# Kernel optimization log

Measured on AMD Instinct MI355X. Metric: run time of the kernel, lower is better.

The kernel has to match this reference:

```python
import jax, jax.numpy as jnp
import numpy as np

N = 50000      # nodes
E = 800000     # edges (avg degree 16)
IN = 128       # in_channels
H = 8          # heads (layer 1)
C = 32         # hidden_channels per head
OUT = 40       # out_channels + 1
NEG_SLOPE = 0.2  # PyG GATConv default


def glorot(key, shape, fan_in, fan_out):
    lim = np.sqrt(6.0 / (fan_in + fan_out)).astype(np.float32)
    return jax.random.uniform(key, shape, jnp.float32, -lim, lim)


def setup_inputs() -> dict:
    key = jax.random.key(0)
    ks = jax.random.split(key, 10)
    x = jax.random.normal(ks[0], (N, IN), jnp.float32)
    edge_index = jax.random.randint(ks[1], (2, E), 0, N, dtype=jnp.int32)
    # layer 1: in -> H*C, heads=8, concat
    W1 = glorot(ks[2], (IN, H * C), IN, H * C)
    att_src1 = glorot(ks[3], (H, C), C, C)
    att_dst1 = glorot(ks[4], (H, C), C, C)
    b1 = jnp.zeros((H * C,), jnp.float32)
    # layer 2: H*C -> OUT, heads=1
    W2 = glorot(ks[5], (H * C, OUT), H * C, OUT)
    att_src2 = glorot(ks[6], (1, OUT), OUT, OUT)
    att_dst2 = glorot(ks[7], (1, OUT), OUT, OUT)
    b2 = jnp.zeros((OUT,), jnp.float32)
    return {"x": x, "edge_index": edge_index, "W1": W1, "att_src1": att_src1,
            "att_dst1": att_dst1, "b1": b1, "W2": W2, "att_src2": att_src2,
            "att_dst2": att_dst2, "b2": b2}


def gat_conv(x, edge_index, W, att_src, att_dst, bias):
    # PyG GATConv (eval mode, add_self_loops=True, concat=True)
    n = x.shape[0]
    heads, ch = att_src.shape
    loop = jnp.arange(n, dtype=edge_index.dtype)
    src = jnp.concatenate([edge_index[0], loop])  # message source j
    dst = jnp.concatenate([edge_index[1], loop])  # message target i
    h = (x @ W).reshape(n, heads, ch)                       # [N,H,C]
    a_src = jnp.einsum('nhc,hc->nh', h, att_src)            # [N,H]
    a_dst = jnp.einsum('nhc,hc->nh', h, att_dst)            # [N,H]
    logits = jax.nn.leaky_relu(a_src[src] + a_dst[dst], NEG_SLOPE)  # [Et,H]
    # segmented softmax over incoming edges of each target node
    m = jax.ops.segment_max(logits, dst, num_segments=n)    # [N,H]
    p = jnp.exp(logits - m[dst])
    s = jax.ops.segment_sum(p, dst, num_segments=n)         # [N,H]
    alpha = p / s[dst]                                      # [Et,H]
    msg = h[src] * alpha[:, :, None]                        # [Et,H,C]
    out = jax.ops.segment_sum(msg, dst, num_segments=n)     # [N,H,C]
    return out.reshape(n, heads * ch) + bias


def reference(x, edge_index, W1, att_src1, att_dst1, b1, W2, att_src2, att_dst2, b2):
    h = gat_conv(x, edge_index, W1, att_src1, att_dst1, b1)
    h = jax.nn.relu(h)  # dropout is identity in eval mode
    h = gat_conv(h, edge_index, W2, att_src2, att_dst2, b2)
    return jax.nn.log_softmax(h, axis=1)
```

## Files before the change

kernel.cpp:

```cpp
#include <hip/hip_runtime.h>
#include <hip/hip_bf16.h>
#include <math.h>

#define NEG_SLOPE 0.2f

__device__ __forceinline__ float lrelu(float x){ return x > 0.f ? x : NEG_SLOPE * x; }
__device__ __forceinline__ unsigned short f2bf(float f){
  __hip_bfloat16 h = __float2bfloat16(f);
  return __builtin_bit_cast(unsigned short, h);
}
__device__ __forceinline__ float b2f(unsigned short u){
  return __builtin_bit_cast(float, (unsigned)u << 16);
}

typedef short bf16x8 __attribute__((ext_vector_type(8)));
typedef float f32x4 __attribute__((ext_vector_type(4)));

__global__ void k_count(const int* __restrict__ dst, int* __restrict__ deg, int E){
  int e = blockIdx.x*256 + threadIdx.x;
  if (e < E) atomicAdd(&deg[dst[e]], 1);
}

__global__ __launch_bounds__(256) void k_scan1(const int* __restrict__ deg, int* __restrict__ bsum, int n){
  int tid = threadIdx.x;
  int base = blockIdx.x*1024 + tid*4;
  int s = 0;
  #pragma unroll
  for (int j=0;j<4;j++){ int idx = base+j; if (idx < n) s += deg[idx]; }
  #pragma unroll
  for (int off=32; off; off>>=1) s += __shfl_xor(s, off);
  __shared__ int ws[4];
  if ((tid&63)==0) ws[tid>>6] = s;
  __syncthreads();
  if (tid==0) bsum[blockIdx.x] = ws[0]+ws[1]+ws[2]+ws[3];
}

__global__ void k_scan2(const int* __restrict__ bsum, int* __restrict__ boff,
                        int* __restrict__ rowptr, int nb, int n){
  int lane = threadIdx.x;
  int v = (lane < nb) ? bsum[lane] : 0;
  int inc = v;
  #pragma unroll
  for (int off=1; off<64; off<<=1){ int t = __shfl_up(inc, off); if (lane >= off) inc += t; }
  if (lane < nb) boff[lane] = inc - v;
  if (lane == 63) rowptr[n] = inc;
}

__global__ __launch_bounds__(256) void k_scan3(const int* __restrict__ deg, const int* __restrict__ boff,
    int* __restrict__ rowptr, int* __restrict__ nxt, int n){
  int tid = threadIdx.x; int lane = tid & 63, w = tid >> 6;
  int base = blockIdx.x*1024 + tid*4;
  int v[4]; int s = 0;
  #pragma unroll
  for (int j=0;j<4;j++){ int idx = base+j; v[j] = (idx < n) ? deg[idx] : 0; s += v[j]; }
  int inc = s;
  #pragma unroll
  for (int off=1; off<64; off<<=1){ int t = __shfl_up(inc, off); if (lane >= off) inc += t; }
  __shared__ int ws[4];
  if (lane == 63) ws[w] = inc;
  __syncthreads();
  int run = boff[blockIdx.x];
  for (int ww=0; ww<w; ww++) run += ws[ww];
  run += inc - s;
  #pragma unroll
  for (int j=0;j<4;j++){ int idx = base+j; if (idx < n){ rowptr[idx] = run; nxt[idx] = run; run += v[j]; } }
}

__global__ void k_scatter(const int* __restrict__ src, const int* __restrict__ dst,
                          int* __restrict__ nxt, int* __restrict__ srcs,
                          int* __restrict__ dsts, int E){
  int e = blockIdx.x*256 + threadIdx.x;
  if (e < E){
    int d = dst[e];
    int pos = atomicAdd(&nxt[d], 1);
    srcs[pos] = src[e];
    dsts[pos] = d;
  }
}

__global__ __launch_bounds__(256) void k_wt2(const float* __restrict__ W1, unsigned short* __restrict__ W1t,
                                             const float* __restrict__ W2, unsigned short* __restrict__ W2t){
  int b = blockIdx.x, tid = threadIdx.x;
  if (b < 128){
    int c = b*2 + (tid>>7), k = tid & 127;
    W1t[(size_t)c*128 + k] = f2bf(W1[(size_t)k*256 + c]);
  } else {
    int c = b - 128, k = tid;
    float v = (c < 40) ? W2[(size_t)k*40 + c] : 0.f;
    W2t[(size_t)c*256 + k] = f2bf(v);
  }
}

__global__ void k_edgep1(const int* __restrict__ srcs, const int* __restrict__ dsts,
    const float* __restrict__ asrc, const float* __restrict__ adst,
    unsigned short* __restrict__ p1, int E8){
  int id = blockIdx.x*256 + threadIdx.x;
  if (id >= E8) return;
  int pos = id >> 3, hd = id & 7;
  int s = srcs[pos], d = dsts[pos];
  float l = lrelu(asrc[(size_t)s*8 + hd] + adst[(size_t)d*8 + hd]);
  p1[id] = f2bf(__expf(l));
}

__global__ void k_edgep2(const int* __restrict__ srcs, const int* __restrict__ dsts,
    const float* __restrict__ asrc, const float* __restrict__ adst,
    float* __restrict__ p2, int E){
  int pos = blockIdx.x*256 + threadIdx.x;
  if (pos >= E) return;
  int s = srcs[pos], d = dsts[pos];
  p2[pos] = __expf(lrelu(asrc[s] + adst[d]));
}

__global__ __launch_bounds__(256) void gemm1_att(
    const float* __restrict__ x, const unsigned short* __restrict__ Bt,
    unsigned short* __restrict__ C, const float* __restrict__ att_s,
    const float* __restrict__ att_d, float* __restrict__ asrc,
    float* __restrict__ adst, int M){
  __shared__ unsigned short sA[64][40];
  __shared__ unsigned short sB[256][40];
  const int tid = threadIdx.x;
  const int wid = tid >> 6, lane = tid & 63;
  const int r0 = blockIdx.x * 64;
  const int fr = lane & 15, fk = (lane >> 4) * 8;
  f32x4 acc[4][4] = {};

  for (int k0 = 0; k0 < 128; k0 += 32){
    #pragma unroll
    for (int t=0; t<2; t++){
      int id = tid + t*256;
      int r = id >> 3, q = id & 7;
      float4 v = make_float4(0.f,0.f,0.f,0.f);
      int row = r0 + r;
      if (row < M) v = ((const float4*)(x + (size_t)row*128))[(k0>>2) + q];
      ushort4 o; o.x=f2bf(v.x); o.y=f2bf(v.y); o.z=f2bf(v.z); o.w=f2bf(v.w);
      *(ushort4*)&sA[r][q*4] = o;
    }
    #pragma unroll
    for (int t=0; t<4; t++){
      int id = tid + t*256;
      int r = id >> 2, lk = (id & 3) * 8;
      uint4 vb = *(const uint4*)(Bt + (size_t)r*128 + k0 + lk);
      *(uint4*)&sB[r][lk] = vb;
    }
    __syncthreads();
    bf16x8 a[4], b[4];
    #pragma unroll
    for (int mi=0; mi<4; mi++) a[mi] = *(const bf16x8*)&sA[mi*16 + fr][fk];
    #pragma unroll
    for (int ni=0; ni<4; ni++) b[ni] = *(const bf16x8*)&sB[wid*64 + ni*16 + fr][fk];
    #pragma unroll
    for (int mi=0; mi<4; mi++)
      #pragma unroll
      for (int ni=0; ni<4; ni++)
        acc[mi][ni] = __builtin_amdgcn_mfma_f32_16x16x32_bf16(a[mi], b[ni], acc[mi][ni], 0,0,0);
    __syncthreads();
  }

  float avs[4], avd[4];
  #pragma unroll
  for (int ni=0; ni<4; ni++){
    int idx = (2*wid + (ni>>1))*32 + (ni&1)*16 + fr;
    avs[ni] = att_s[idx];
    avd[ni] = att_d[idx];
  }

  #pragma unroll
  for (int mi=0; mi<4; mi++){
    #pragma unroll
    for (int j=0; j<4; j++){
      int row = r0 + mi*16 + (lane>>4)*4 + j;
      #pragma unroll
      for (int ni=0; ni<4; ni++){
        int col = wid*64 + ni*16 + fr;
        if (row < M) C[(size_t)row*256 + col] = f2bf(acc[mi][ni][j]);
      }
      float s0 = acc[mi][0][j]*avs[0] + acc[mi][1][j]*avs[1];
      float s1 = acc[mi][2][j]*avs[2] + acc[mi][3][j]*avs[3];
      float d0 = acc[mi][0][j]*avd[0] + acc[mi][1][j]*avd[1];
      float d1 = acc[mi][2][j]*avd[2] + acc[mi][3][j]*avd[3];
      #pragma unroll
      for (int mk=1; mk<16; mk<<=1){
        s0 += __shfl_xor(s0, mk); s1 += __shfl_xor(s1, mk);
        d0 += __shfl_xor(d0, mk); d1 += __shfl_xor(d1, mk);
      }
      if ((lane & 15) == 0 && row < M){
        asrc[(size_t)row*8 + 2*wid    ] = s0;
        asrc[(size_t)row*8 + 2*wid + 1] = s1;
        adst[(size_t)row*8 + 2*wid    ] = d0;
        adst[(size_t)row*8 + 2*wid + 1] = d1;
      }
    }
  }
}

__global__ __launch_bounds__(256) void gemm2_att(
    const unsigned short* __restrict__ A, const unsigned short* __restrict__ Bt,
    unsigned short* __restrict__ C, const float* __restrict__ att_s,
    const float* __restrict__ att_d, float* __restrict__ asrc,
    float* __restrict__ adst, int M){
  __shared__ unsigned short sA[64][40];
  __shared__ unsigned short sB[64][40];
  __shared__ float sS[2][64], sD[2][64];
  const int tid = threadIdx.x;
  const int wid = tid >> 6, lane = tid & 63;
  const int r0 = blockIdx.x * 64;
  const int wr = wid >> 1, wc = wid & 1;
  const int lr = tid >> 2;
  const int lk = (tid & 3) * 8;
  const int fr = lane & 15, fk = (lane >> 4) * 8;
  const int K = 256;
  f32x4 acc[2][2] = {};

  for (int k0 = 0; k0 < K; k0 += 32){
    uint4 va = make_uint4(0,0,0,0);
    int row = r0 + lr;
    if (row < M) va = *(const uint4*)(A + (size_t)row*K + k0 + lk);
    *(uint4*)&sA[lr][lk] = va;
    uint4 vb = *(const uint4*)(Bt + (size_t)lr*K + k0 + lk);
    *(uint4*)&sB[lr][lk] = vb;
    __syncthreads();
    bf16x8 a0 = *(const bf16x8*)&sA[wr*32 + fr][fk];
    bf16x8 a1 = *(const bf16x8*)&sA[wr*32 + 16 + fr][fk];
    bf16x8 b0 = *(const bf16x8*)&sB[wc*32 + fr][fk];
    bf16x8 b1 = *(const bf16x8*)&sB[wc*32 + 16 + fr][fk];
    acc[0][0] = __builtin_amdgcn_mfma_f32_16x16x32_bf16(a0, b0, acc[0][0], 0,0,0);
    acc[0][1] = __builtin_amdgcn_mfma_f32_16x16x32_bf16(a0, b1, acc[0][1], 0,0,0);
    acc[1][0] = __builtin_amdgcn_mfma_f32_16x16x32_bf16(a1, b0, acc[1][0], 0,0,0);
    acc[1][1] = __builtin_amdgcn_mfma_f32_16x16x32_bf16(a1, b1, acc[1][1], 0,0,0);
    __syncthreads();
  }

  float avs[2], avd[2];
  #pragma unroll
  for (int ni=0; ni<2; ni++){
    int col = wc*32 + ni*16 + fr;
    avs[ni] = (col < 40) ? att_s[col] : 0.f;
    avd[ni] = (col < 40) ? att_d[col] : 0.f;
  }

  #pragma unroll
  for (int mi=0; mi<2; mi++){
    #pragma unroll
    for (int j=0;j<4;j++){
      int lrow = wr*32 + mi*16 + (lane>>4)*4 + j;
      int row = r0 + lrow;
      #pragma unroll
      for (int ni=0; ni<2; ni++){
        int col = wc*32 + ni*16 + fr;
        if (row < M) C[(size_t)row*64 + col] = f2bf(acc[mi][ni][j]);
      }
      float s = acc[mi][0][j]*avs[0] + acc[mi][1][j]*avs[1];
      float d = acc[mi][0][j]*avd[0] + acc[mi][1][j]*avd[1];
      #pragma unroll
      for (int mk=1; mk<16; mk<<=1){
        s += __shfl_xor(s, mk); d += __shfl_xor(d, mk);
      }
      if ((lane & 15) == 0){ sS[wc][lrow] = s; sD[wc][lrow] = d; }
    }
  }
  __syncthreads();
  if (tid < 64){
    int row = r0 + tid;
    if (row < M){
      asrc[row] = sS[0][tid] + sS[1][tid];
      adst[row] = sD[0][tid] + sD[1][tid];
    }
  }
}

__global__ __launch_bounds__(256) void k_agg1(
    const unsigned short* __restrict__ h1, const float* __restrict__ asrc,
    const float* __restrict__ adst, const int* __restrict__ rowptr,
    const int* __restrict__ srcs, const unsigned short* __restrict__ p1,
    const float* __restrict__ bias, unsigned short* __restrict__ zb, int n){
  int gw = (blockIdx.x*256 + threadIdx.x) >> 6;
  int lane = threadIdx.x & 63;
  int i = gw >> 1, half = gw & 1;
  if (i >= n) return;
  int hd = half*4 + (lane >> 4);
  float pself = __expf(lrelu(asrc[(size_t)i*8 + hd] + adst[(size_t)i*8 + hd]));
  float ssum = pself;
  unsigned hv = ((const unsigned*)(h1 + (size_t)i*256))[half*64 + lane];
  float accx = pself * b2f((unsigned short)(hv & 0xffff));
  float accy = pself * b2f((unsigned short)(hv >> 16));
  int e0 = rowptr[i], e1 = rowptr[i+1];
  int efull = e0 + ((e1 - e0) & ~7);
  for (int e = e0; e < efull; e += 8){
    int sx[8]; unsigned vv[8]; float pv[8];
    #pragma unroll
    for (int j=0;j<8;j++) sx[j] = srcs[e+j];
    #pragma unroll
    for (int j=0;j<8;j++) vv[j] = ((const unsigned*)(h1 + (size_t)sx[j]*256))[half*64 + lane];
    #pragma unroll
    for (int j=0;j<8;j++) pv[j] = b2f(p1[(size_t)(e+j)*8 + hd]);
    #pragma unroll
    for (int j=0;j<8;j++){
      float p = pv[j];
      ssum += p;
      accx += p * b2f((unsigned short)(vv[j] & 0xffff));
      accy += p * b2f((unsigned short)(vv[j] >> 16));
    }
  }
  if (efull < e1){
    int sx[8]; unsigned vv[8]; float pv[8];
    #pragma unroll
    for (int j=0;j<8;j++){
      int ee = efull + j;
      int idx = ee < e1 ? ee : e1 - 1;
      sx[j] = srcs[idx];
      unsigned short pr = p1[(size_t)idx*8 + hd];
      pv[j] = (ee < e1) ? b2f(pr) : 0.f;
    }
    #pragma unroll
    for (int j=0;j<8;j++) vv[j] = ((const unsigned*)(h1 + (size_t)sx[j]*256))[half*64 + lane];
    #pragma unroll
    for (int j=0;j<8;j++){
      float p = pv[j];
      ssum += p;
      accx += p * b2f((unsigned short)(vv[j] & 0xffff));
      accy += p * b2f((unsigned short)(vv[j] >> 16));
    }
  }
  float inv = 1.f / ssum;
  float2 b = ((const float2*)bias)[half*64 + lane];
  unsigned ob = (unsigned)f2bf(fmaxf(fmaf(accx, inv, b.x), 0.f))
              | ((unsigned)f2bf(fmaxf(fmaf(accy, inv, b.y), 0.f)) << 16);
  ((unsigned*)(zb + (size_t)i*256))[half*64 + lane] = ob;
}

__global__ __launch_bounds__(256) void k_agg2(
    const unsigned short* __restrict__ h2, const float* __restrict__ asrc,
    const float* __restrict__ adst, const int* __restrict__ rowptr,
    const int* __restrict__ srcs, const float* __restrict__ p2,
    const float* __restrict__ bias, float* __restrict__ out, int n){
  int wid = (blockIdx.x*256 + threadIdx.x) >> 6;
  int lane = threadIdx.x & 63;
  if (wid >= n) return;
  int i = wid;
  bool act = lane < 40;
  float pself = __expf(lrelu(asrc[i] + adst[i]));
  float ssum = pself;
  float acc = pself * b2f(h2[(size_t)i*64 + lane]);
  int e0 = rowptr[i], e1 = rowptr[i+1];
  int efull = e0 + ((e1 - e0) & ~7);
  for (int e = e0; e < efull; e += 8){
    int sx[8]; float vv[8], pv[8];
    #pragma unroll
    for (int j=0;j<8;j++) sx[j] = srcs[e+j];
    #pragma unroll
    for (int j=0;j<8;j++) vv[j] = b2f(h2[(size_t)sx[j]*64 + lane]);
    #pragma unroll
    for (int j=0;j<8;j++) pv[j] = p2[e+j];
    #pragma unroll
    for (int j=0;j<8;j++){
      ssum += pv[j];
      acc += pv[j] * vv[j];
    }
  }
  if (efull < e1){
    int sx[8]; float vv[8], pv[8];
    #pragma unroll
    for (int j=0;j<8;j++){
      int ee = efull + j;
      int idx = ee < e1 ? ee : e1 - 1;
      sx[j] = srcs[idx];
      float pr = p2[idx];
      pv[j] = (ee < e1) ? pr : 0.f;
    }
    #pragma unroll
    for (int j=0;j<8;j++) vv[j] = b2f(h2[(size_t)sx[j]*64 + lane]);
    #pragma unroll
    for (int j=0;j<8;j++){
      ssum += pv[j];
      acc += pv[j] * vv[j];
    }
  }
  float val = act ? (acc/ssum + bias[lane]) : -INFINITY;
  float mx = val;
  #pragma unroll
  for (int off=32; off; off>>=1) mx = fmaxf(mx, __shfl_xor(mx, off));
  float ex = act ? __expf(val - mx) : 0.f;
  float se = ex;
  #pragma unroll
  for (int off=32; off; off>>=1) se += __shfl_xor(se, off);
  if (act) out[(size_t)i*40 + lane] = val - mx - __logf(se);
}

extern "C" void kernel_launch(void* const* d_in, const int* in_sizes, int n_in,
                              void* d_out, int out_size, void* d_ws, size_t ws_size,
                              hipStream_t stream){
  const float* x   = (const float*)d_in[0];
  const int*   ei  = (const int*)d_in[1];
  const float* W1  = (const float*)d_in[2];
  const float* as1 = (const float*)d_in[3];
  const float* ad1 = (const float*)d_in[4];
  const float* b1  = (const float*)d_in[5];
  const float* W2  = (const float*)d_in[6];
  const float* as2 = (const float*)d_in[7];
  const float* ad2 = (const float*)d_in[8];
  const float* b2  = (const float*)d_in[9];
  float* out = (float*)d_out;

  const int N = in_sizes[0] / 128;
  const int E = in_sizes[1] / 2;
  const int* srcI = ei;
  const int* dstI = ei + E;

  char* ws = (char*)d_ws;
  size_t off = 0;
  auto alloc = [&](size_t bytes){ void* p = ws + off; off += (bytes + 255) & ~(size_t)255; return p; };
  unsigned short* h1b = (unsigned short*)alloc((size_t)N*256*2);
  unsigned short* zb  = (unsigned short*)alloc((size_t)N*256*2);
  unsigned short* h2b = (unsigned short*)alloc((size_t)N*64*2);
  unsigned short* W1t = (unsigned short*)alloc((size_t)256*128*2);
  unsigned short* W2t = (unsigned short*)alloc((size_t)64*256*2);
  unsigned short* p1  = (unsigned short*)alloc((size_t)E*8*2);
  float* p2    = (float*)alloc((size_t)E*4);
  float* asrc1 = (float*)alloc((size_t)N*8*4);
  float* adst1 = (float*)alloc((size_t)N*8*4);
  float* asrc2 = (float*)alloc((size_t)N*4);
  float* adst2 = (float*)alloc((size_t)N*4);
  int* deg     = (int*)alloc((size_t)N*4);
  int* rowptr  = (int*)alloc((size_t)(N+1)*4);
  int* nxt     = (int*)alloc((size_t)N*4);
  int* srcs    = (int*)alloc((size_t)E*4);
  int* dsts    = (int*)alloc((size_t)E*4);
  int* bsum    = (int*)alloc(256*4);
  int* boff    = (int*)alloc(256*4);
  (void)ws_size; (void)n_in; (void)out_size;

  const int nb = (N + 1023)/1024;
  hipMemsetAsync(deg, 0, (size_t)N*4, stream);
  int eb = (E + 255)/256;
  k_count <<<eb, 256, 0, stream>>>(dstI, deg, E);
  k_scan1 <<<nb, 256, 0, stream>>>(deg, bsum, N);
  k_scan2 <<<1, 64, 0, stream>>>(bsum, boff, rowptr, nb, N);
  k_scan3 <<<nb, 256, 0, stream>>>(deg, boff, rowptr, nxt, N);
  k_scatter<<<eb, 256, 0, stream>>>(srcI, dstI, nxt, srcs, dsts, E);

  k_wt2<<<192, 256, 0, stream>>>(W1, W1t, W2, W2t);

  gemm1_att<<<(N + 63)/64, 256, 0, stream>>>(x, W1t, h1b, as1, ad1, asrc1, adst1, N);
  k_edgep1<<<(E*8 + 255)/256, 256, 0, stream>>>(srcs, dsts, asrc1, adst1, p1, E*8);
  k_agg1<<<(2*N + 3)/4, 256, 0, stream>>>(h1b, asrc1, adst1, rowptr, srcs, p1, b1, zb, N);

  gemm2_att<<<(N + 63)/64, 256, 0, stream>>>(zb, W2t, h2b, as2, ad2, asrc2, adst2, N);
  k_edgep2<<<eb, 256, 0, stream>>>(srcs, dsts, asrc2, adst2, p2, E);
  k_agg2<<<(N + 3)/4, 256, 0, stream>>>(h2b, asrc2, adst2, rowptr, srcs, p2, b2, out, N);
}
```

Baseline: 337.1 us.

## Merge setup kernels, drop dsts array, and restructure edge and aggregation kernels

Fuses the degree count with the weight transpose, and folds the single-block scan into the final scan kernel, which cuts the number of launches. The CSR scatter no longer writes a per-edge dst array. Edge-probability kernels now walk rows by node, so adst is read once per node. The aggregation kernels use one wave per node with two half-waves handling alternating edges and wide uint4 gathers, combined by a cross-half shuffle. This removes launches and dst traffic at the cost of idle lanes on low-degree nodes and some extra shuffle work.

```diff
diff --git a/kernel.cpp b/kernel.cpp
--- a/kernel.cpp
+++ b/kernel.cpp
@@ -9,16 +9,34 @@
   __hip_bfloat16 h = __float2bfloat16(f);
   return __builtin_bit_cast(unsigned short, h);
 }
-__device__ __forceinline__ float b2f(unsigned short u){
-  return __builtin_bit_cast(float, (unsigned)u << 16);
+__device__ __forceinline__ float b2f(unsigned u){
+  return __builtin_bit_cast(float, u << 16);
+}
+__device__ __forceinline__ float b2fh(unsigned u){
+  return __builtin_bit_cast(float, u & 0xffff0000u);
 }
 
 typedef short bf16x8 __attribute__((ext_vector_type(8)));
 typedef float f32x4 __attribute__((ext_vector_type(4)));
 
-__global__ void k_count(const int* __restrict__ dst, int* __restrict__ deg, int E){
-  int e = blockIdx.x*256 + threadIdx.x;
-  if (e < E) atomicAdd(&deg[dst[e]], 1);
+__global__ void k_count_wt(const int* __restrict__ dst, int* __restrict__ deg, int E, int eb,
+                           const float* __restrict__ W1, unsigned short* __restrict__ W1t,
+                           const float* __restrict__ W2, unsigned short* __restrict__ W2t){
+  int b = blockIdx.x, tid = threadIdx.x;
+  if (b < eb){
+    int e = b*256 + tid;
+    if (e < E) atomicAdd(&deg[dst[e]], 1);
+  } else {
+    int bb = b - eb;
+    if (bb < 128){
+      int c = bb*2 + (tid>>7), k = tid & 127;
+      W1t[(size_t)c*128 + k] = f2bf(W1[(size_t)k*256 + c]);
+    } else {
+      int c = bb - 128, k = tid;
+      float v = (c < 40) ? W2[(size_t)k*40 + c] : 0.f;
+      W2t[(size_t)c*256 + k] = f2bf(v);
+    }
+  }
 }
 
 __global__ __launch_bounds__(256) void k_scan1(const int* __restrict__ deg, int* __restrict__ bsum, int n){
@@ -35,20 +53,20 @@
   if (tid==0) bsum[blockIdx.x] = ws[0]+ws[1]+ws[2]+ws[3];
 }
 
-__global__ void k_scan2(const int* __restrict__ bsum, int* __restrict__ boff,
-                        int* __restrict__ rowptr, int nb, int n){
-  int lane = threadIdx.x;
-  int v = (lane < nb) ? bsum[lane] : 0;
-  int inc = v;
-  #pragma unroll
-  for (int off=1; off<64; off<<=1){ int t = __shfl_up(inc, off); if (lane >= off) inc += t; }
-  if (lane < nb) boff[lane] = inc - v;
-  if (lane == 63) rowptr[n] = inc;
-}
-
-__global__ __launch_bounds__(256) void k_scan3(const int* __restrict__ deg, const int* __restrict__ boff,
-    int* __restrict__ rowptr, int* __restrict__ nxt, int n){
+__global__ __launch_bounds__(256) void k_scan3(const int* __restrict__ deg, const int* __restrict__ bsum,
+    int* __restrict__ rowptr, int* __restrict__ nxt, int n, int nb){
   int tid = threadIdx.x; int lane = tid & 63, w = tid >> 6;
+  __shared__ int ws[4];
+  __shared__ int s_boff;
+  if (tid < 64){
+    int v = (lane < nb) ? bsum[lane] : 0;
+    int inc = v;
+    #pragma unroll
+    for (int off=1; off<64; off<<=1){ int t = __shfl_up(inc, off); if (lane >= off) inc += t; }
+    if (lane == blockIdx.x) s_boff = inc - v;
+    if (blockIdx.x == 0 && lane == nb-1) rowptr[n] = inc;
+  }
+  __syncthreads();
   int base = blockIdx.x*1024 + tid*4;
   int v[4]; int s = 0;
   #pragma unroll
@@ -56,10 +74,9 @@
   int inc = s;
   #pragma unroll
   for (int off=1; off<64; off<<=1){ int t = __shfl_up(inc, off); if (lane >= off) inc += t; }
-  __shared__ int ws[4];
   if (lane == 63) ws[w] = inc;
   __syncthreads();
-  int run = boff[blockIdx.x];
+  int run = s_boff;
   for (int ww=0; ww<w; ww++) run += ws[ww];
   run += inc - s;
   #pragma unroll
@@ -67,48 +84,40 @@
 }
 
 __global__ void k_scatter(const int* __restrict__ src, const int* __restrict__ dst,
-                          int* __restrict__ nxt, int* __restrict__ srcs,
-                          int* __restrict__ dsts, int E){
+                          int* __restrict__ nxt, int* __restrict__ srcs, int E){
   int e = blockIdx.x*256 + threadIdx.x;
   if (e < E){
-    int d = dst[e];
-    int pos = atomicAdd(&nxt[d], 1);
+    int pos = atomicAdd(&nxt[dst[e]], 1);
     srcs[pos] = src[e];
-    dsts[pos] = d;
-  }
-}
-
-__global__ __launch_bounds__(256) void k_wt2(const float* __restrict__ W1, unsigned short* __restrict__ W1t,
-                                             const float* __restrict__ W2, unsigned short* __restrict__ W2t){
-  int b = blockIdx.x, tid = threadIdx.x;
-  if (b < 128){
-    int c = b*2 + (tid>>7), k = tid & 127;
-    W1t[(size_t)c*128 + k] = f2bf(W1[(size_t)k*256 + c]);
-  } else {
-    int c = b - 128, k = tid;
-    float v = (c < 40) ? W2[(size_t)k*40 + c] : 0.f;
-    W2t[(size_t)c*256 + k] = f2bf(v);
-  }
-}
-
-__global__ void k_edgep1(const int* __restrict__ srcs, const int* __restrict__ dsts,
-    const float* __restrict__ asrc, const float* __restrict__ adst,
-    unsigned short* __restrict__ p1, int E8){
-  int id = blockIdx.x*256 + threadIdx.x;
-  if (id >= E8) return;
-  int pos = id >> 3, hd = id & 7;
-  int s = srcs[pos], d = dsts[pos];
-  float l = lrelu(asrc[(size_t)s*8 + hd] + adst[(size_t)d*8 + hd]);
-  p1[id] = f2bf(__expf(l));
-}
-
-__global__ void k_edgep2(const int* __restrict__ srcs, const int* __restrict__ dsts,
-    const float* __restrict__ asrc, const float* __restrict__ adst,
-    float* __restrict__ p2, int E){
-  int pos = blockIdx.x*256 + threadIdx.x;
-  if (pos >= E) return;
-  int s = srcs[pos], d = dsts[pos];
-  p2[pos] = __expf(lrelu(asrc[s] + adst[d]));
+  }
+}
+
+__global__ __launch_bounds__(256) void k_edgep1n(const int* __restrict__ rowptr,
+    const int* __restrict__ srcs, const float* __restrict__ asrc,
+    const float* __restrict__ adst, unsigned short* __restrict__ p1, int n){
+  int i = (blockIdx.x*256 + threadIdx.x) >> 6;
+  int lane = threadIdx.x & 63;
+  if (i >= n) return;
+  int hd = lane & 7, eoff = lane >> 3;
+  float ad = adst[(size_t)i*8 + hd];
+  int e0 = rowptr[i], e1 = rowptr[i+1];
+  for (int e = e0 + eoff; e < e1; e += 8){
+    int s = srcs[e];
+    p1[(size_t)e*8 + hd] = f2bf(__expf(lrelu(asrc[(size_t)s*8 + hd] + ad)));
+  }
+}
+
+__global__ __launch_bounds__(256) void k_edgep2n(const int* __restrict__ rowptr,
+    const int* __restrict__ srcs, const float* __restrict__ asrc,
+    const float* __restrict__ adst, float* __restrict__ p2, int n){
+  int i = (blockIdx.x*256 + threadIdx.x) >> 6;
+  int lane = threadIdx.x & 63;
+  if (i >= n) return;
+  float ad = adst[i];
+  int e0 = rowptr[i], e1 = rowptr[i+1];
+  for (int e = e0 + lane; e < e1; e += 64){
+    p2[e] = __expf(lrelu(asrc[srcs[e]] + ad));
+  }
 }
 
 __global__ __launch_bounds__(256) void gemm1_att(
@@ -273,59 +282,79 @@
     const float* __restrict__ adst, const int* __restrict__ rowptr,
     const int* __restrict__ srcs, const unsigned short* __restrict__ p1,
     const float* __restrict__ bias, unsigned short* __restrict__ zb, int n){
-  int gw = (blockIdx.x*256 + threadIdx.x) >> 6;
+  int i = (blockIdx.x*256 + threadIdx.x) >> 6;
   int lane = threadIdx.x & 63;
-  int i = gw >> 1, half = gw & 1;
   if (i >= n) return;
-  int hd = half*4 + (lane >> 4);
-  float pself = __expf(lrelu(asrc[(size_t)i*8 + hd] + adst[(size_t)i*8 + hd]));
-  float ssum = pself;
-  unsigned hv = ((const unsigned*)(h1 + (size_t)i*256))[half*64 + lane];
-  float accx = pself * b2f((unsigned short)(hv & 0xffff));
-  float accy = pself * b2f((unsigned short)(hv >> 16));
+  int half = lane >> 5, l32 = lane & 31;
+  int hd = l32 >> 2;
+  float acc[8] = {0.f,0.f,0.f,0.f,0.f,0.f,0.f,0.f};
+  float ssum = 0.f;
+  if (half == 0){
+    float pself = __expf(lrelu(asrc[(size_t)i*8 + hd] + adst[(size_t)i*8 + hd]));
+    uint4 hv = ((const uint4*)(h1 + (size_t)i*256))[l32];
+    acc[0]=pself*b2f(hv.x&0xffff); acc[1]=pself*b2fh(hv.x);
+    acc[2]=pself*b2f(hv.y&0xffff); acc[3]=pself*b2fh(hv.y);
+    acc[4]=pself*b2f(hv.z&0xffff); acc[5]=pself*b2fh(hv.z);
+    acc[6]=pself*b2f(hv.w&0xffff); acc[7]=pself*b2fh(hv.w);
+    ssum = pself;
+  }
   int e0 = rowptr[i], e1 = rowptr[i+1];
-  int efull = e0 + ((e1 - e0) & ~7);
-  for (int e = e0; e < efull; e += 8){
-    int sx[8]; unsigned vv[8]; float pv[8];
-    #pragma unroll
-    for (int j=0;j<8;j++) sx[j] = srcs[e+j];
-    #pragma unroll
-    for (int j=0;j<8;j++) vv[j] = ((const unsigned*)(h1 + (size_t)sx[j]*256))[half*64 + lane];
-    #pragma unroll
-    for (int j=0;j<8;j++) pv[j] = b2f(p1[(size_t)(e+j)*8 + hd]);
-    #pragma unroll
-    for (int j=0;j<8;j++){
-      float p = pv[j];
-      ssum += p;
-      accx += p * b2f((unsigned short)(vv[j] & 0xffff));
-      accy += p * b2f((unsigned short)(vv[j] >> 16));
-    }
-  }
-  if (efull < e1){
-    int sx[8]; unsigned vv[8]; float pv[8];
-    #pragma unroll
-    for (int j=0;j<8;j++){
-      int ee = efull + j;
-      int idx = ee < e1 ? ee : e1 - 1;
-      sx[j] = srcs[idx];
-      unsigned short pr = p1[(size_t)idx*8 + hd];
-      pv[j] = (ee < e1) ? b2f(pr) : 0.f;
-    }
-    #pragma unroll
-    for (int j=0;j<8;j++) vv[j] = ((const unsigned*)(h1 + (size_t)sx[j]*256))[half*64 + lane];
-    #pragma unroll
-    for (int j=0;j<8;j++){
-      float p = pv[j];
-      ssum += p;
-      accx += p * b2f((unsigned short)(vv[j] & 0xffff));
-      accy += p * b2f((unsigned short)(vv[j] >> 16));
-    }
-  }
-  float inv = 1.f / ssum;
-  float2 b = ((const float2*)bias)[half*64 + lane];
-  unsigned ob = (unsigned)f2bf(fmaxf(fmaf(accx, inv, b.x), 0.f))
-              | ((unsigned)f2bf(fmaxf(fmaf(accy, inv, b.y), 0.f)) << 16);
-  ((unsigned*)(zb + (size_t)i*256))[half*64 + lane] = ob;
+  int nume = e1 - e0;
+  int full = nume & ~7;
+  for (int eo = 0; eo < full; eo += 8){
+    int sx[4]; float pv[4];
+    #pragma unroll
+    for (int j=0;j<4;j++){
+      int e = e0 + eo + 2*j + half;
+      sx[j] = srcs[e];
+      pv[j] = b2f((unsigned)p1[(size_t)e*8 + hd]);
+    }
+    uint4 vv[4];
+    #pragma unroll
+    for (int j=0;j<4;j++) vv[j] = ((const uint4*)(h1 + (size_t)sx[j]*256))[l32];
+    #pragma unroll
+    for (int j=0;j<4;j++){
+      float p = pv[j]; ssum += p;
+      acc[0]+=p*b2f(vv[j].x&0xffff); acc[1]+=p*b2fh(vv[j].x);
+      acc[2]+=p*b2f(vv[j].y&0xffff); acc[3]+=p*b2fh(vv[j].y);
+      acc[4]+=p*b2f(vv[j].z&0xffff); acc[5]+=p*b2fh(vv[j].z);
+      acc[6]+=p*b2f(vv[j].w&0xffff); acc[7]+=p*b2fh(vv[j].w);
+    }
+  }
+  for (int eo = full; eo < nume; eo += 2){
+    int idx = eo + half;
+    bool ok = idx < nume;
+    int e = e0 + (ok ? idx : 0);
+    float p = ok ? b2f((unsigned)p1[(size_t)e*8 + hd]) : 0.f;
+    uint4 v = ((const uint4*)(h1 + (size_t)srcs[e]*256))[l32];
+    ssum += p;
+    acc[0]+=p*b2f(v.x&0xffff); acc[1]+=p*b2fh(v.x);
+    acc[2]+=p*b2f(v.y&0xffff); acc[3]+=p*b2fh(v.y);
+    acc[4]+=p*b2f(v.z&0xffff); acc[5]+=p*b2fh(v.z);
+    acc[6]+=p*b2f(v.w&0xffff); acc[7]+=p*b2fh(v.w);
+  }
+  ssum += __shfl_xor(ssum, 32);
+  #pragma unroll
+  for (int c=0;c<8;c++) acc[c] += __shfl_xor(acc[c], 32);
+  if (half == 0){
+    float inv = 1.f / ssum;
+    float4 b0 = ((const float4*)bias)[l32*2];
+    float4 b1 = ((const float4*)bias)[l32*2 + 1];
+    unsigned short o0 = f2bf(fmaxf(fmaf(acc[0], inv, b0.x), 0.f));
+    unsigned short o1 = f2bf(fmaxf(fmaf(acc[1], inv, b0.y), 0.f));
+    unsigned short o2 = f2bf(fmaxf(fmaf(acc[2], inv, b0.z), 0.f));
+    unsigned short o3 = f2bf(fmaxf(fmaf(acc[3], inv, b0.w), 0.f));
+    unsigned short o4 = f2bf(fmaxf(fmaf(acc[4], inv, b1.x), 0.f));
+    unsigned short o5 = f2bf(fmaxf(fmaf(acc[5], inv, b1.y), 0.f));
+    unsigned short o6 = f2bf(fmaxf(fmaf(acc[6], inv, b1.z), 0.f));
+    unsigned short o7 = f2bf(fmaxf(fmaf(acc[7], inv, b1.w), 0.f));
+    uint4 ov;
+    ov.x = (unsigned)o0 | ((unsigned)o1 << 16);
+    ov.y = (unsigned)o2 | ((unsigned)o3 << 16);
+    ov.z = (unsigned)o4 | ((unsigned)o5 << 16);
+    ov.w = (unsigned)o6 | ((unsigned)o7 << 16);
+    ((uint4*)(zb + (size_t)i*256))[l32] = ov;
+  }
 }
 
 __global__ __launch_bounds__(256) void k_agg2(
@@ -333,57 +362,68 @@
     const float* __restrict__ adst, const int* __restrict__ rowptr,
     const int* __restrict__ srcs, const float* __restrict__ p2,
     const float* __restrict__ bias, float* __restrict__ out, int n){
-  int wid = (blockIdx.x*256 + threadIdx.x) >> 6;
+  int i = (blockIdx.x*256 + threadIdx.x) >> 6;
   int lane = threadIdx.x & 63;
-  if (wid >= n) return;
-  int i = wid;
-  bool act = lane < 40;
-  float pself = __expf(lrelu(asrc[i] + adst[i]));
-  float ssum = pself;
-  float acc = pself * b2f(h2[(size_t)i*64 + lane]);
+  if (i >= n) return;
+  int half = lane >> 5, l32 = lane & 31;
+  int c0 = l32*2;
+  bool act = l32 < 20;
+  float acc0 = 0.f, acc1 = 0.f, ssum = 0.f;
+  if (half == 0){
+    float pself = __expf(lrelu(asrc[i] + adst[i]));
+    unsigned hv = ((const unsigned*)(h2 + (size_t)i*64))[l32];
+    acc0 = pself * b2f(hv & 0xffff);
+    acc1 = pself * b2fh(hv);
+    ssum = pself;
+  }
   int e0 = rowptr[i], e1 = rowptr[i+1];
-  int efull = e0 + ((e1 - e0) & ~7);
-  for (int e = e0; e < efull; e += 8){
-    int sx[8]; float vv[8], pv[8];
-    #pragma unroll
-    for (int j=0;j<8;j++) sx[j] = srcs[e+j];
-    #pragma unroll
-    for (int j=0;j<8;j++) vv[j] = b2f(h2[(size_t)sx[j]*64 + lane]);
-    #pragma unroll
-    for (int j=0;j<8;j++) pv[j] = p2[e+j];
-    #pragma unroll
-    for (int j=0;j<8;j++){
-      ssum += pv[j];
-      acc += pv[j] * vv[j];
-    }
-  }
-  if (efull < e1){
-    int sx[8]; float vv[8], pv[8];
-    #pragma unroll
-    for (int j=0;j<8;j++){
-      int ee = efull + j;
-      int idx = ee < e1 ? ee : e1 - 1;
-      sx[j] = srcs[idx];
-      float pr = p2[idx];
-      pv[j] = (ee < e1) ? pr : 0.f;
-    }
-    #pragma unroll
-    for (int j=0;j<8;j++) vv[j] = b2f(h2[(size_t)sx[j]*64 + lane]);
-    #pragma unroll
-    for (int j=0;j<8;j++){
-      ssum += pv[j];
-      acc += pv[j] * vv[j];
-    }
-  }
-  float val = act ? (acc/ssum + bias[lane]) : -INFINITY;
-  float mx = val;
+  int nume = e1 - e0;
+  int full = nume & ~7;
+  for (int eo = 0; eo < full; eo += 8){
+    int sx[4]; float pv[4];
+    #pragma unroll
+    for (int j=0;j<4;j++){
+      int e = e0 + eo + 2*j + half;
+      sx[j] = srcs[e];
+      pv[j] = p2[e];
+    }
+    unsigned vv[4];
+    #pragma unroll
+    for (int j=0;j<4;j++) vv[j] = ((const unsigned*)(h2 + (size_t)sx[j]*64))[l32];
+    #pragma unroll
+    for (int j=0;j<4;j++){
+      float p = pv[j]; ssum += p;
+      acc0 += p * b2f(vv[j] & 0xffff);
+      acc1 += p * b2fh(vv[j]);
+    }
+  }
+  for (int eo = full; eo < nume; eo += 2){
+    int idx = eo + half;
+    bool ok = idx < nume;
+    int e = e0 + (ok ? idx : 0);
+    float p = ok ? p2[e] : 0.f;
+    unsigned v = ((const unsigned*)(h2 + (size_t)srcs[e]*64))[l32];
+    ssum += p;
+    acc0 += p * b2f(v & 0xffff);
+    acc1 += p * b2fh(v);
+  }
+  ssum += __shfl_xor(ssum, 32);
+  acc0 += __shfl_xor(acc0, 32);
+  acc1 += __shfl_xor(acc1, 32);
+  float inv = 1.f / ssum;
+  float v0 = act ? (acc0*inv + bias[c0])   : -INFINITY;
+  float v1 = act ? (acc1*inv + bias[c0+1]) : -INFINITY;
+  float mx = fmaxf(v0, v1);
   #pragma unroll
   for (int off=32; off; off>>=1) mx = fmaxf(mx, __shfl_xor(mx, off));
-  float ex = act ? __expf(val - mx) : 0.f;
-  float se = ex;
-  #pragma unroll
-  for (int off=32; off; off>>=1) se += __shfl_xor(se, off);
-  if (act) out[(size_t)i*40 + lane] = val - mx - __logf(se);
+  float ex = (half == 0 && act) ? (__expf(v0 - mx) + __expf(v1 - mx)) : 0.f;
+  #pragma unroll
+  for (int off=32; off; off>>=1) ex += __shfl_xor(ex, off);
+  if (half == 0 && act){
+    float ls = __logf(ex);
+    float2 o; o.x = v0 - mx - ls; o.y = v1 - mx - ls;
+    ((float2*)(out + (size_t)i*40))[l32] = o;
+  }
 }
 
 extern "C" void kernel_launch(void* const* d_in, const int* in_sizes, int n_in,
@@ -424,27 +464,22 @@
   int* rowptr  = (int*)alloc((size_t)(N+1)*4);
   int* nxt     = (int*)alloc((size_t)N*4);
   int* srcs    = (int*)alloc((size_t)E*4);
-  int* dsts    = (int*)alloc((size_t)E*4);
   int* bsum    = (int*)alloc(256*4);
-  int* boff    = (int*)alloc(256*4);
   (void)ws_size; (void)n_in; (void)out_size;
 
   const int nb = (N + 1023)/1024;
+  const int eb = (E + 255)/256;
   hipMemsetAsync(deg, 0, (size_t)N*4, stream);
-  int eb = (E + 255)/256;
-  k_count <<<eb, 256, 0, stream>>>(dstI, deg, E);
+  k_count_wt<<<eb + 192, 256, 0, stream>>>(dstI, deg, E, eb, W1, W1t, W2, W2t);
   k_scan1 <<<nb, 256, 0, stream>>>(deg, bsum, N);
-  k_scan2 <<<1, 64, 0, stream>>>(bsum, boff, rowptr, nb, N);
-  k_scan3 <<<nb, 256, 0, stream>>>(deg, boff, rowptr, nxt, N);
-  k_scatter<<<eb, 256, 0, stream>>>(srcI, dstI, nxt, srcs, dsts, E);
-
-  k_wt2<<<192, 256, 0, stream>>>(W1, W1t, W2, W2t);
+  k_scan3 <<<nb, 256, 0, stream>>>(deg, bsum, rowptr, nxt, N, nb);
+  k_scatter<<<eb, 256, 0, stream>>>(srcI, dstI, nxt, srcs, E);
 
   gemm1_att<<<(N + 63)/64, 256, 0, stream>>>(x, W1t, h1b, as1, ad1, asrc1, adst1, N);
-  k_edgep1<<<(E*8 + 255)/256, 256, 0, stream>>>(srcs, dsts, asrc1, adst1, p1, E*8);
-  k_agg1<<<(2*N + 3)/4, 256, 0, stream>>>(h1b, asrc1, adst1, rowptr, srcs, p1, b1, zb, N);
+  k_edgep1n<<<(N + 3)/4, 256, 0, stream>>>(rowptr, srcs, asrc1, adst1, p1, N);
+  k_agg1<<<(N + 3)/4, 256, 0, stream>>>(h1b, asrc1, adst1, rowptr, srcs, p1, b1, zb, N);
 
   gemm2_att<<<(N + 63)/64, 256, 0, stream>>>(zb, W2t, h2b, as2, ad2, asrc2, adst2, N);
-  k_edgep2<<<eb, 256, 0, stream>>>(srcs, dsts, asrc2, adst2, p2, E);
+  k_edgep2n<<<(N + 3)/4, 256, 0, stream>>>(rowptr, srcs, asrc2, adst2, p2, N);
   k_agg2<<<(N + 3)/4, 256, 0, stream>>>(h2b, asrc2, adst2, rowptr, srcs, p2, b2, out, N);
 }
```

New measurement: 332.1 us. Within noise of the previous version (-1.5%).
